# Kernel tuning notes

Hardware: AMD Instinct MI355X
Metric: run time of the kernel (lower is better)

Reference implementation:

```python
import jax, jax.numpy as jnp
import numpy as np

B, S, D, M = 2, 4096, 128, 64

def _linear_init(key, shape, fan_in):
    bound = 1.0 / np.sqrt(fan_in)
    return jax.random.uniform(key, shape, jnp.float32, -bound, bound)

def setup_inputs() -> dict:
    key = jax.random.key(0)
    ks = jax.random.split(key, 18)
    x = jax.random.normal(ks[0], (B, S, D), jnp.float32)
    context = jax.random.normal(ks[1], (B, S, D), jnp.float32)
    # per-mechanism params (torch Linear semantics: y = x @ W.T + b)
    Wt = _linear_init(ks[2], (M, D, D), D)   # transform weight, laid out [m, in, out]
    bt = _linear_init(ks[3], (M, D), D)
    char = jax.random.normal(ks[4], (M, D), jnp.float32)  # characteristics [1,1,d] per mech
    Wg = _linear_init(ks[5], (M, D), D)      # timing_gate weight (out=1)
    bg = _linear_init(ks[6], (M,), D)
    Wv = _linear_init(ks[7], (M, D), D)      # victory_detector weight (out=1)
    bv = _linear_init(ks[8], (M,), D)
    O = jax.random.normal(ks[9], (M, M), jnp.float32) * 0.02  # overcoming matrix
    # selector: Linear(2D,2D) -> GELU -> Linear(2D,M)
    W1 = _linear_init(ks[10], (2 * D, 2 * D), 2 * D)
    b1 = _linear_init(ks[11], (2 * D,), 2 * D)
    W2 = _linear_init(ks[12], (2 * D, M), 2 * D)
    b2 = _linear_init(ks[13], (M,), 2 * D)
    # integrate: Linear(2D, D)
    Wi = _linear_init(ks[14], (2 * D, D), 2 * D)
    bi = _linear_init(ks[15], (D,), 2 * D)
    return {"x": x, "context": context, "Wt": Wt, "bt": bt, "char": char,
            "Wg": Wg, "bg": bg, "Wv": Wv, "bv": bv, "O": O,
            "W1": W1, "b1": b1, "W2": W2, "b2": b2, "Wi": Wi, "bi": bi}

def reference(x, context, Wt, bt, char, Wg, bg, Wv, bv, O, W1, b1, W2, b2, Wi, bi):
    # selection scores over mechanisms
    sel_in = jnp.concatenate([x, context], axis=-1)          # [b,s,2d]
    h = jax.nn.gelu(sel_in @ W1 + b1, approximate=False)
    selection_scores = jax.nn.softmax(h @ W2 + b2, axis=-1)  # [b,s,m]
    # all 64 mechanism nodes as one batched GEMM
    transformed = jnp.einsum('bsd,mde->bsme', x, Wt) + bt + char   # [b,s,m,d]
    timing = jax.nn.sigmoid(jnp.einsum('bsd,md->bsm', x, Wg) + bg)  # [b,s,m]
    victory = jax.nn.sigmoid(jnp.einsum('bsme,me->bsm', transformed, Wv) + bv)
    outputs = transformed * timing[..., None]                # [b,s,m,d]
    # strategic overcoming modulation: gate = 1 + tanh(scores @ O)
    gates = 1.0 + jnp.tanh(selection_scores @ O)             # [b,s,m]
    selected = jnp.einsum('bsme,bsm->bse', outputs, gates * selection_scores)
    victory_potential = jnp.sum(victory * selection_scores, axis=-1)  # [b,s]
    integrated = jnp.concatenate([x, selected], axis=-1) @ Wi + bi    # [b,s,d]
    return integrated, victory_potential
```

## Files before the change

### kernel.cpp

```cpp
#include <hip/hip_runtime.h>
#include <hip/hip_bf16.h>


typedef __bf16 bf16_t;
typedef __bf16 bf16x8 __attribute__((ext_vector_type(8)));
typedef float  f32x4  __attribute__((ext_vector_type(4)));

#define WS_WTT      0u
#define WS_W1T      2097152u
#define WS_W2T      2228224u
#define WS_OT       2260992u
#define WS_WG       2269184u
#define WS_U        2285568u
#define WS_CVEC     2301952u
#define WS_BCT      2302208u
#define WS_WIT      2318592u
#define WS_WT       2384128u
#define WS_SBIAS    4481280u
#define WS_SEL0     8675584u
#define WS_SEL1     12869888u

#define VP_OFF 1048576

__device__ __forceinline__ f32x4 mfma16(bf16x8 a, bf16x8 b, f32x4 c) {
  return __builtin_amdgcn_mfma_f32_16x16x32_bf16(a, b, c, 0, 0, 0);
}

__device__ __forceinline__ float erf_fast(float x) {
  float ax = fabsf(x);
  float t = 1.0f / (1.0f + 0.3275911f * ax);
  float p = t * (0.254829592f + t * (-0.284496736f + t * (1.421413741f +
            t * (-1.453152027f + t * 1.061405429f))));
  float y = 1.0f - p * __expf(-ax * ax);
  return copysignf(y, x);
}
__device__ __forceinline__ float gelu_fast(float v) {
  return 0.5f * v * (1.0f + erf_fast(v * 0.70710678118654752f));
}
__device__ __forceinline__ float tanh_fast(float x) {
  float xc = fminf(fmaxf(x, -15.f), 15.f);
  float e = __expf(2.0f * xc);
  return (e - 1.0f) / (e + 1.0f);
}
__device__ __forceinline__ float sigmoidf_(float v) {
  return 1.0f / (1.0f + __expf(-v));
}

__device__ __forceinline__ bf16x8 cvt8(float4 v0, float4 v1) {
  bf16x8 a;
  a[0] = (bf16_t)v0.x; a[1] = (bf16_t)v0.y; a[2] = (bf16_t)v0.z; a[3] = (bf16_t)v0.w;
  a[4] = (bf16_t)v1.x; a[5] = (bf16_t)v1.y; a[6] = (bf16_t)v1.z; a[7] = (bf16_t)v1.w;
  return a;
}

__global__ __launch_bounds__(256) void kprep(
    const float* __restrict__ Wt, const float* __restrict__ bt,
    const float* __restrict__ ch, const float* __restrict__ Wg,
    const float* __restrict__ Wv, const float* __restrict__ bv,
    const float* __restrict__ O, const float* __restrict__ W1,
    const float* __restrict__ W2, const float* __restrict__ Wi,
    char* __restrict__ ws)
{
  const int bid = blockIdx.x, tid = threadIdx.x;
  if (bid < 128) {
    const int m = bid >> 1, half = bid & 1;
    const float* wtm = Wt + m * 16384;
    bf16_t* wtt = (bf16_t*)(ws + WS_WTT) + m * 16384;
    const int ks = half * 2 + (tid >> 7), e = tid & 127;
    bf16_t tmp[32];
    #pragma unroll
    for (int dd = 0; dd < 32; ++dd)
      tmp[dd] = (bf16_t)wtm[(ks * 32 + dd) * 128 + e];
    bf16_t* dst = wtt + ks * 4096 + e * 32;
    #pragma unroll
    for (int g = 0; g < 4; ++g)
      *(bf16x8*)(dst + g * 8) = *(const bf16x8*)(tmp + g * 8);
  } else if (bid < 144) {
    int base = (bid - 128) * 256 + tid;
    int k = base >> 4, c0 = (base & 15) * 16;
    bf16_t* o = (bf16_t*)(ws + WS_W1T);
    #pragma unroll
    for (int j = 0; j < 16; ++j) o[(c0 + j) * 256 + k] = (bf16_t)W1[k * 256 + c0 + j];
  } else if (bid < 146) {
    int base = (bid - 144) * 256 + tid;
    int k = base >> 1, c0 = (base & 1) * 32;
    bf16_t* o = (bf16_t*)(ws + WS_W2T);
    #pragma unroll
    for (int j = 0; j < 32; ++j) o[(c0 + j) * 256 + k] = (bf16_t)W2[k * 64 + c0 + j];
  } else if (bid == 146) {
    int k = tid >> 2, c0 = (tid & 3) * 16;
    bf16_t* o = (bf16_t*)(ws + WS_OT);
    #pragma unroll
    for (int j = 0; j < 16; ++j) o[(c0 + j) * 64 + k] = (bf16_t)O[k * 64 + c0 + j];
  } else if (bid == 147) {
    bf16_t* o = (bf16_t*)(ws + WS_WG);
    #pragma unroll
    for (int j = 0; j < 32; ++j) o[tid * 32 + j] = (bf16_t)Wg[tid * 32 + j];
  } else if (bid == 148) {
    bf16_t* o = (bf16_t*)(ws + WS_BCT);
    #pragma unroll
    for (int i = 0; i < 4; ++i) {
      int task = tid + i * 256;
      int m = task >> 4, e0 = (task & 15) * 8;
      #pragma unroll
      for (int j = 0; j < 8; ++j)
        o[(e0 + j) * 64 + m] = (bf16_t)(bt[m * 128 + e0 + j] + ch[m * 128 + e0 + j]);
    }
  } else if (bid < 153) {
    int base = (bid - 149) * 256 + tid;
    int k = base >> 2, c0 = (base & 3) * 32;
    bf16_t* o = (bf16_t*)(ws + WS_WIT);
    #pragma unroll
    for (int j = 0; j < 32; ++j) o[(c0 + j) * 256 + k] = (bf16_t)Wi[k * 128 + c0 + j];
  } else if (bid < 185) {
    int task = (bid - 153) * 256 + tid;
    int m = task >> 7, d = task & 127;
    const float4* wp = (const float4*)(Wt + m * 16384 + d * 128);
    const float4* vp = (const float4*)(Wv + m * 128);
    float s = 0.f;
    #pragma unroll
    for (int i = 0; i < 32; ++i) {
      float4 a = wp[i], b = vp[i];
      s += a.x * b.x + a.y * b.y + a.z * b.z + a.w * b.w;
    }
    ((bf16_t*)(ws + WS_U))[m * 128 + d] = (bf16_t)s;
  } else {
    if (tid < 64) {
      int m = tid;
      const float4* bp = (const float4*)(bt + m * 128);
      const float4* cp = (const float4*)(ch + m * 128);
      const float4* vp = (const float4*)(Wv + m * 128);
      float s = bv[m];
      #pragma unroll
      for (int i = 0; i < 32; ++i) {
        float4 a = bp[i], c = cp[i], b = vp[i];
        s += (a.x + c.x) * b.x + (a.y + c.y) * b.y + (a.z + c.z) * b.z + (a.w + c.w) * b.w;
      }
      ((float*)(ws + WS_CVEC))[m] = s;
    }
  }
}

__global__ __launch_bounds__(256) void kselect(
    const float* __restrict__ x, const float* __restrict__ ctx,
    const float* __restrict__ b1, const float* __restrict__ b2,
    const float* __restrict__ bg,
    char* __restrict__ ws, float* __restrict__ out)
{
  __shared__ char sm[43008];
  bf16_t* hL      = (bf16_t*)sm;
  float*  scoresL = (float*)(sm + 16384);
  float*  wLT     = (float*)(sm + 24576);
  bf16_t* scbL    = (bf16_t*)(sm + 33792);
  bf16_t* wbL     = (bf16_t*)(sm + 37888);
  float*  vpL     = (float*)(sm + 41984);

  const int tid = threadIdx.x;
  const int lane = tid & 63, wq = tid >> 6;
  const int tb = blockIdx.x * 32;
  const int lr = lane & 15, lg = lane >> 4;
  const int lk = lg * 8, lj4 = lg * 4;

  const bf16_t* W1t = (const bf16_t*)(ws + WS_W1T);
  const bf16_t* W2t = (const bf16_t*)(ws + WS_W2T);
  const bf16_t* Ot  = (const bf16_t*)(ws + WS_OT);
  const bf16_t* Wgb = (const bf16_t*)(ws + WS_WG);
  const bf16_t* Ub  = (const bf16_t*)(ws + WS_U);
  const float*  cv  = (const float*)(ws + WS_CVEC);
  const bf16_t* bct = (const bf16_t*)(ws + WS_BCT);
  float* wT    = (float*)(ws + WS_WT);
  float* sbOut = (float*)(ws + WS_SBIAS);

  bf16x8 aX[2][4];
  #pragma unroll
  for (int rg = 0; rg < 2; ++rg) {
    const float* xr = x + (tb + rg * 16 + lr) * 128;
    #pragma unroll
    for (int ks = 0; ks < 4; ++ks)
      aX[rg][ks] = cvt8(*(const float4*)(xr + ks * 32 + lk),
                        *(const float4*)(xr + ks * 32 + lk + 4));
  }

  {
    f32x4 a1[4][2] = {{{0,0,0,0},{0,0,0,0}},{{0,0,0,0},{0,0,0,0}},
                      {{0,0,0,0},{0,0,0,0}},{{0,0,0,0},{0,0,0,0}}};
    #pragma unroll
    for (int ks = 0; ks < 8; ++ks) {
      bf16x8 af[2];
      if (ks < 4) {
        af[0] = aX[0][ks]; af[1] = aX[1][ks];
      } else {
        #pragma unroll
        for (int rg = 0; rg < 2; ++rg) {
          const float* cr = ctx + (tb + rg * 16 + lr) * 128 + (ks - 4) * 32 + lk;
          af[rg] = cvt8(*(const float4*)cr, *(const float4*)(cr + 4));
        }
      }
      #pragma unroll
      for (int cg = 0; cg < 4; ++cg) {
        bf16x8 b = *(const bf16x8*)(W1t + (wq * 64 + cg * 16 + lr) * 256 + ks * 32 + lk);
        a1[cg][0] = mfma16(af[0], b, a1[cg][0]);
        a1[cg][1] = mfma16(af[1], b, a1[cg][1]);
      }
    }
    #pragma unroll
    for (int cg = 0; cg < 4; ++cg) {
      int c = wq * 64 + cg * 16 + lr;
      float bb = b1[c];
      #pragma unroll
      for (int rg = 0; rg < 2; ++rg)
        #pragma unroll
        for (int j = 0; j < 4; ++j) {
          int r = rg * 16 + lj4 + j;
          float v = gelu_fast(a1[cg][rg][j] + bb);
          *(bf16_t*)((char*)hL + ((r * 512 + c * 2) ^ ((r & 7) << 4))) = (bf16_t)v;
        }
    }
  }
  __syncthreads();

  {
    int c = wq * 16 + lr;
    f32x4 l[2] = {{0,0,0,0},{0,0,0,0}};
    #pragma unroll
    for (int ks = 0; ks < 8; ++ks) {
      int k0 = ks * 32 + lk;
      bf16x8 b = *(const bf16x8*)(W2t + c * 256 + k0);
      #pragma unroll
      for (int rg = 0; rg < 2; ++rg) {
        int r = rg * 16 + lr;
        bf16x8 a = *(const bf16x8*)((char*)hL + ((r * 512 + k0 * 2) ^ ((r & 7) << 4)));
        l[rg] = mfma16(a, b, l[rg]);
      }
    }
    float bb = b2[c];
    #pragma unroll
    for (int rg = 0; rg < 2; ++rg)
      #pragma unroll
      for (int j = 0; j < 4; ++j)
        scoresL[(rg * 16 + lj4 + j) * 64 + c] = l[rg][j] + bb;
  }
  __syncthreads();

  {
    int row = tid >> 3, i = tid & 7;
    float v[8];
    #pragma unroll
    for (int j = 0; j < 8; ++j) v[j] = scoresL[row * 64 + i * 8 + j];
    float mx = v[0];
    #pragma unroll
    for (int j = 1; j < 8; ++j) mx = fmaxf(mx, v[j]);
    mx = fmaxf(mx, __shfl_xor(mx, 1));
    mx = fmaxf(mx, __shfl_xor(mx, 2));
    mx = fmaxf(mx, __shfl_xor(mx, 4));
    float sum = 0.f;
    #pragma unroll
    for (int j = 0; j < 8; ++j) { v[j] = __expf(v[j] - mx); sum += v[j]; }
    sum += __shfl_xor(sum, 1);
    sum += __shfl_xor(sum, 2);
    sum += __shfl_xor(sum, 4);
    float inv = 1.0f / sum;
    #pragma unroll
    for (int j = 0; j < 8; ++j) {
      float s = v[j] * inv;
      int cc = i * 8 + j;
      scoresL[row * 64 + cc] = s;
      *(bf16_t*)((char*)scbL + ((row * 128 + cc * 2) ^ ((row & 7) << 4))) = (bf16_t)s;
    }
  }
  __syncthreads();

  {
    const int c = wq * 16 + lr;
    f32x4 g[2] = {{0,0,0,0},{0,0,0,0}};
    #pragma unroll
    for (int ks = 0; ks < 2; ++ks) {
      int k0 = ks * 32 + lk;
      bf16x8 b = *(const bf16x8*)(Ot + c * 64 + k0);
      #pragma unroll
      for (int rg = 0; rg < 2; ++rg) {
        int r = rg * 16 + lr;
        bf16x8 a = *(const bf16x8*)((char*)scbL + ((r * 128 + k0 * 2) ^ ((r & 7) << 4)));
        g[rg] = mfma16(a, b, g[rg]);
      }
    }
    f32x4 t[2] = {{0,0,0,0},{0,0,0,0}};
    f32x4 v[2] = {{0,0,0,0},{0,0,0,0}};
    #pragma unroll
    for (int ks = 0; ks < 4; ++ks) {
      bf16x8 bT = *(const bf16x8*)(Wgb + c * 128 + ks * 32 + lk);
      bf16x8 bV = *(const bf16x8*)(Ub  + c * 128 + ks * 32 + lk);
      #pragma unroll
      for (int rg = 0; rg < 2; ++rg) {
        t[rg] = mfma16(aX[rg][ks], bT, t[rg]);
        v[rg] = mfma16(aX[rg][ks], bV, v[rg]);
      }
    }
    float bgc = bg[c], cvc = cv[c];
    #pragma unroll
    for (int rg = 0; rg < 2; ++rg)
      #pragma unroll
      for (int j = 0; j < 4; ++j) {
        int r = rg * 16 + lj4 + j;
        float gate = 1.0f + tanh_fast(g[rg][j]);
        float tim  = sigmoidf_(t[rg][j] + bgc);
        float vic  = sigmoidf_(v[rg][j] + cvc);
        float sc   = scoresL[r * 64 + c];
        float w    = gate * sc * tim;
        wLT[c * 36 + r] = w;
        *(bf16_t*)((char*)wbL + ((r * 128 + c * 2) ^ ((r & 7) << 4))) = (bf16_t)w;
        float pv = vic * sc;
        pv += __shfl_xor(pv, 1); pv += __shfl_xor(pv, 2);
        pv += __shfl_xor(pv, 4); pv += __shfl_xor(pv, 8);
        if (lr == 0) vpL[r * 4 + wq] = pv;
      }
  }
  __syncthreads();

  if (tid < 32) {
    float s = vpL[tid * 4 + 0] + vpL[tid * 4 + 1] + vpL[tid * 4 + 2] + vpL[tid * 4 + 3];
    out[VP_OFF + tb + tid] = s;
  }
  {
    int m = tid >> 2, r0 = (tid & 3) * 8;
    float4 v0 = *(const float4*)&wLT[m * 36 + r0];
    float4 v1 = *(const float4*)&wLT[m * 36 + r0 + 4];
    *(float4*)&wT[m * 8192 + tb + r0] = v0;
    *(float4*)&wT[m * 8192 + tb + r0 + 4] = v1;
  }
  #pragma unroll
  for (int cg = 0; cg < 2; ++cg) {
    int eg = wq * 32 + cg * 16 + lr;
    f32x4 s[2] = {{0,0,0,0},{0,0,0,0}};
    #pragma unroll
    for (int ks = 0; ks < 2; ++ks) {
      int k0 = ks * 32 + lk;
      bf16x8 b = *(const bf16x8*)(bct + eg * 64 + k0);
      #pragma unroll
      for (int rg = 0; rg < 2; ++rg) {
        int r = rg * 16 + lr;
        bf16x8 a = *(const bf16x8*)((char*)wbL + ((r * 128 + k0 * 2) ^ ((r & 7) << 4)));
        s[rg] = mfma16(a, b, s[rg]);
      }
    }
    #pragma unroll
    for (int rg = 0; rg < 2; ++rg)
      #pragma unroll
      for (int j = 0; j < 4; ++j)
        sbOut[(tb + rg * 16 + lj4 + j) * 128 + eg] = s[rg][j];
  }
}

__device__ __forceinline__ void loadF(bf16x8 (&F)[4], const char* bbase, int mm) {
  const char* p = bbase + mm * 32768;
  F[0] = *(const bf16x8*)(p);
  F[1] = *(const bf16x8*)(p + 8192);
  F[2] = *(const bf16x8*)(p + 16384);
  F[3] = *(const bf16x8*)(p + 24576);
}

__device__ __forceinline__ void stepM(const bf16x8 (&F)[4], const float* wrow,
                                      const bf16x8 (&aX)[4][4], f32x4 (&acc)[4], int lj4) {
  f32x4 y[4] = {{0,0,0,0},{0,0,0,0},{0,0,0,0},{0,0,0,0}};
  #pragma unroll
  for (int ks = 0; ks < 4; ++ks) {
    y[0] = mfma16(aX[0][ks], F[ks], y[0]);
    y[1] = mfma16(aX[1][ks], F[ks], y[1]);
    y[2] = mfma16(aX[2][ks], F[ks], y[2]);
    y[3] = mfma16(aX[3][ks], F[ks], y[3]);
  }
  #pragma unroll
  for (int rg = 0; rg < 4; ++rg) {
    f32x4 wv = *(const f32x4*)(wrow + rg * 16 + lj4);
    #pragma unroll
    for (int jj = 0; jj < 4; ++jj)
      acc[rg][jj] += wv[jj] * y[rg][jj];
  }
}

__global__ __launch_bounds__(256, 2) void kmech(
    const float* __restrict__ x, char* __restrict__ ws)
{
  __shared__ float wmT[32 * 68];
  const int tid = threadIdx.x;
  const int lane = tid & 63, wq = tid >> 6;
  const int b = blockIdx.x;
  const int tile = b >> 2, eh = (b >> 1) & 1, mh = b & 1;
  const int tb = tile * 64;
  const int lr = lane & 15, lg = lane >> 4;
  const int lk = lg * 8, lj4 = lg * 4;

  const char* wttc = (const char*)(ws + WS_WTT);
  const float* wT = (const float*)(ws + WS_WT);
  float* selOut = (float*)(ws + (mh ? WS_SEL1 : WS_SEL0));

  {
    int mm = tid >> 3, r0 = (tid & 7) * 8;
    const float* src = wT + (mh * 32 + mm) * 8192 + tb + r0;
    float4 a = *(const float4*)src, c = *(const float4*)(src + 4);
    *(float4*)&wmT[mm * 68 + r0] = a;
    *(float4*)&wmT[mm * 68 + r0 + 4] = c;
  }
  bf16x8 aX[4][4];
  #pragma unroll
  for (int rg = 0; rg < 4; ++rg) {
    const float* xr = x + (tb + rg * 16 + lr) * 128;
    #pragma unroll
    for (int ks = 0; ks < 4; ++ks)
      aX[rg][ks] = cvt8(*(const float4*)(xr + ks * 32 + lk),
                        *(const float4*)(xr + ks * 32 + lk + 4));
  }
  f32x4 acc[4] = {{0,0,0,0},{0,0,0,0},{0,0,0,0},{0,0,0,0}};
  __syncthreads();

  const char* bbase = wttc + (size_t)(mh * 32) * 32768
                    + (size_t)(((eh * 64 + wq * 16 + lr) * 32 + lg * 8) * 2);
  bf16x8 F0[4], F1[4], F2[4], F3[4];
  loadF(F0, bbase, 0);
  loadF(F1, bbase, 1);
  loadF(F2, bbase, 2);

  #pragma unroll
  for (int it = 0; it < 8; ++it) {
    const int base = it * 4;
    const int n3 = base + 3;
    const int n4 = base + 4 > 31 ? 31 : base + 4;
    const int n5 = base + 5 > 31 ? 31 : base + 5;
    const int n6 = base + 6 > 31 ? 31 : base + 6;
    loadF(F3, bbase, n3);
    stepM(F0, &wmT[(base + 0) * 68], aX, acc, lj4);
    loadF(F0, bbase, n4);
    stepM(F1, &wmT[(base + 1) * 68], aX, acc, lj4);
    loadF(F1, bbase, n5);
    stepM(F2, &wmT[(base + 2) * 68], aX, acc, lj4);
    loadF(F2, bbase, n6);
    stepM(F3, &wmT[(base + 3) * 68], aX, acc, lj4);
  }

  #pragma unroll
  for (int rg = 0; rg < 4; ++rg)
    #pragma unroll
    for (int j = 0; j < 4; ++j)
      selOut[(tb + rg * 16 + lj4 + j) * 128 + eh * 64 + wq * 16 + lr] = acc[rg][j];
}

__global__ __launch_bounds__(256) void kinteg(
    const float* __restrict__ x, const float* __restrict__ bi,
    const char* __restrict__ ws, float* __restrict__ out)
{
  const int tid = threadIdx.x;
  const int lane = tid & 63, wq = tid >> 6;
  const int tb = blockIdx.x * 32;
  const int lr = lane & 15, lg = lane >> 4;
  const int lk = lg * 8, lj4 = lg * 4;
  const bf16_t* Wit = (const bf16_t*)(ws + WS_WIT);
  const float* s0 = (const float*)(ws + WS_SEL0);
  const float* s1 = (const float*)(ws + WS_SEL1);
  const float* sb = (const float*)(ws + WS_SBIAS);

  bf16x8 aF[2][8];
  #pragma unroll
  for (int rg = 0; rg < 2; ++rg) {
    int t = tb + rg * 16 + lr;
    #pragma unroll
    for (int ks = 0; ks < 4; ++ks) {
      const float* src = x + t * 128 + ks * 32 + lk;
      aF[rg][ks] = cvt8(*(const float4*)src, *(const float4*)(src + 4));
    }
    #pragma unroll
    for (int ks = 0; ks < 4; ++ks) {
      int idx = t * 128 + ks * 32 + lk;
      float4 a0 = *(const float4*)(s0 + idx);
      float4 a1 = *(const float4*)(s1 + idx);
      float4 a2 = *(const float4*)(sb + idx);
      float4 b0 = *(const float4*)(s0 + idx + 4);
      float4 b1 = *(const float4*)(s1 + idx + 4);
      float4 b2 = *(const float4*)(sb + idx + 4);
      float4 u; u.x = a0.x + a1.x + a2.x; u.y = a0.y + a1.y + a2.y;
      u.z = a0.z + a1.z + a2.z; u.w = a0.w + a1.w + a2.w;
      float4 v; v.x = b0.x + b1.x + b2.x; v.y = b0.y + b1.y + b2.y;
      v.z = b0.z + b1.z + b2.z; v.w = b0.w + b1.w + b2.w;
      aF[rg][4 + ks] = cvt8(u, v);
    }
  }
  #pragma unroll
  for (int cg = 0; cg < 2; ++cg) {
    int c = wq * 32 + cg * 16 + lr;
    f32x4 a0 = {0,0,0,0}, a1 = {0,0,0,0};
    #pragma unroll
    for (int ks = 0; ks < 8; ++ks) {
      bf16x8 b = *(const bf16x8*)(Wit + c * 256 + ks * 32 + lk);
      a0 = mfma16(aF[0][ks], b, a0);
      a1 = mfma16(aF[1][ks], b, a1);
    }
    float bb = bi[c];
    #pragma unroll
    for (int j = 0; j < 4; ++j) {
      out[(tb + lj4 + j) * 128 + c] = a0[j] + bb;
      out[(tb + 16 + lj4 + j) * 128 + c] = a1[j] + bb;
    }
  }
}

extern "C" void kernel_launch(void* const* d_in, const int* in_sizes, int n_in,
                              void* d_out, int out_size, void* d_ws, size_t ws_size,
                              hipStream_t stream)
{
  (void)in_sizes; (void)n_in; (void)out_size; (void)ws_size;
  const float* x   = (const float*)d_in[0];
  const float* ctx = (const float*)d_in[1];
  const float* Wt  = (const float*)d_in[2];
  const float* bt  = (const float*)d_in[3];
  const float* ch  = (const float*)d_in[4];
  const float* Wg  = (const float*)d_in[5];
  const float* bg  = (const float*)d_in[6];
  const float* Wv  = (const float*)d_in[7];
  const float* bv  = (const float*)d_in[8];
  const float* O   = (const float*)d_in[9];
  const float* W1  = (const float*)d_in[10];
  const float* b1  = (const float*)d_in[11];
  const float* W2  = (const float*)d_in[12];
  const float* b2  = (const float*)d_in[13];
  const float* Wi  = (const float*)d_in[14];
  const float* bi  = (const float*)d_in[15];
  float* out = (float*)d_out;
  char* ws = (char*)d_ws;

  kprep<<<186, 256, 0, stream>>>(Wt, bt, ch, Wg, Wv, bv, O, W1, W2, Wi, ws);
  kselect<<<256, 256, 0, stream>>>(x, ctx, b1, b2, bg, ws, out);
  kmech<<<512, 256, 0, stream>>>(x, ws);
  kinteg<<<256, 256, 0, stream>>>(x, bi, ws, out);
}
```

Baseline: 152.7 us.

## Restructure mechanism kernel: larger token tiles, in-block mechanism split-K reduction

```diff
diff --git a/kernel.cpp b/kernel.cpp
--- a/kernel.cpp
+++ b/kernel.cpp
@@ -17,8 +17,7 @@
 #define WS_WIT      2318592u
 #define WS_WT       2384128u
 #define WS_SBIAS    4481280u
-#define WS_SEL0     8675584u
-#define WS_SEL1     12869888u
+#define WS_SEL      8675584u
 
 #define VP_OFF 1048576
 
@@ -351,97 +350,132 @@
   }
 }
 
-__device__ __forceinline__ void loadF(bf16x8 (&F)[4], const char* bbase, int mm) {
-  const char* p = bbase + mm * 32768;
+__device__ __forceinline__ void loadF4(bf16x8 (&F)[4], const char* bbase, int m) {
+  const char* p = bbase + m * 32768;
   F[0] = *(const bf16x8*)(p);
   F[1] = *(const bf16x8*)(p + 8192);
   F[2] = *(const bf16x8*)(p + 16384);
   F[3] = *(const bf16x8*)(p + 24576);
 }
 
-__device__ __forceinline__ void stepM(const bf16x8 (&F)[4], const float* wrow,
-                                      const bf16x8 (&aX)[4][4], f32x4 (&acc)[4], int lj4) {
-  f32x4 y[4] = {{0,0,0,0},{0,0,0,0},{0,0,0,0},{0,0,0,0}};
+__device__ __forceinline__ void loadG(bf16x8 (&F)[4][4], const char* bbase, int mg) {
   #pragma unroll
-  for (int ks = 0; ks < 4; ++ks) {
-    y[0] = mfma16(aX[0][ks], F[ks], y[0]);
-    y[1] = mfma16(aX[1][ks], F[ks], y[1]);
-    y[2] = mfma16(aX[2][ks], F[ks], y[2]);
-    y[3] = mfma16(aX[3][ks], F[ks], y[3]);
-  }
+  for (int j = 0; j < 4; ++j) loadF4(F[j], bbase, mg + j);
+}
+
+__device__ __forceinline__ void groupStep(const bf16x8 (&F)[4][4], int mg,
+                                          const bf16_t* xL, const float* wmT,
+                                          f32x4 (&acc)[8], int lr, int lg, int lj4) {
   #pragma unroll
-  for (int rg = 0; rg < 4; ++rg) {
-    f32x4 wv = *(const f32x4*)(wrow + rg * 16 + lj4);
-    #pragma unroll
-    for (int jj = 0; jj < 4; ++jj)
-      acc[rg][jj] += wv[jj] * y[rg][jj];
-  }
-}
-
-__global__ __launch_bounds__(256, 2) void kmech(
+  for (int rg = 0; rg < 8; ++rg) {
+    const int r = rg * 16 + lr;
+    const int rx = (r & 7) << 4;
+    bf16x8 a0 = *(const bf16x8*)((const char*)xL + ((r * 256 +   0 + lg * 16) ^ rx));
+    bf16x8 a1 = *(const bf16x8*)((const char*)xL + ((r * 256 +  64 + lg * 16) ^ rx));
+    bf16x8 a2 = *(const bf16x8*)((const char*)xL + ((r * 256 + 128 + lg * 16) ^ rx));
+    bf16x8 a3 = *(const bf16x8*)((const char*)xL + ((r * 256 + 192 + lg * 16) ^ rx));
+    #pragma unroll
+    for (int J = 0; J < 4; ++J) {
+      f32x4 y = {0.f, 0.f, 0.f, 0.f};
+      y = mfma16(a0, F[J][0], y);
+      y = mfma16(a1, F[J][1], y);
+      y = mfma16(a2, F[J][2], y);
+      y = mfma16(a3, F[J][3], y);
+      f32x4 wv = *(const f32x4*)(wmT + (mg + J) * 132 + rg * 16 + lj4);
+      #pragma unroll
+      for (int jj = 0; jj < 4; ++jj)
+        acc[rg][jj] += wv[jj] * y[jj];
+    }
+  }
+}
+
+__global__ __launch_bounds__(512, 2) void kmech(
     const float* __restrict__ x, char* __restrict__ ws)
 {
-  __shared__ float wmT[32 * 68];
+  __shared__ char sm[66560];
+  bf16_t* xL  = (bf16_t*)sm;
+  float*  wmT = (float*)(sm + 32768);
+  float*  scr = (float*)sm;
+
   const int tid = threadIdx.x;
-  const int lane = tid & 63, wq = tid >> 6;
-  const int b = blockIdx.x;
-  const int tile = b >> 2, eh = (b >> 1) & 1, mh = b & 1;
-  const int tb = tile * 64;
+  const int lane = tid & 63, wid = tid >> 6;
+  const int es = wid & 1;
+  const int mq = wid >> 1;
+  const int tile = blockIdx.x >> 2, esl = blockIdx.x & 3;
+  const int tb = tile * 128;
   const int lr = lane & 15, lg = lane >> 4;
-  const int lk = lg * 8, lj4 = lg * 4;
-
-  const char* wttc = (const char*)(ws + WS_WTT);
-  const float* wT = (const float*)(ws + WS_WT);
-  float* selOut = (float*)(ws + (mh ? WS_SEL1 : WS_SEL0));
-
-  {
-    int mm = tid >> 3, r0 = (tid & 7) * 8;
-    const float* src = wT + (mh * 32 + mm) * 8192 + tb + r0;
-    float4 a = *(const float4*)src, c = *(const float4*)(src + 4);
-    *(float4*)&wmT[mm * 68 + r0] = a;
-    *(float4*)&wmT[mm * 68 + r0 + 4] = c;
-  }
-  bf16x8 aX[4][4];
-  #pragma unroll
-  for (int rg = 0; rg < 4; ++rg) {
-    const float* xr = x + (tb + rg * 16 + lr) * 128;
-    #pragma unroll
-    for (int ks = 0; ks < 4; ++ks)
-      aX[rg][ks] = cvt8(*(const float4*)(xr + ks * 32 + lk),
-                        *(const float4*)(xr + ks * 32 + lk + 4));
-  }
-  f32x4 acc[4] = {{0,0,0,0},{0,0,0,0},{0,0,0,0},{0,0,0,0}};
-  __syncthreads();
-
-  const char* bbase = wttc + (size_t)(mh * 32) * 32768
-                    + (size_t)(((eh * 64 + wq * 16 + lr) * 32 + lg * 8) * 2);
-  bf16x8 F0[4], F1[4], F2[4], F3[4];
-  loadF(F0, bbase, 0);
-  loadF(F1, bbase, 1);
-  loadF(F2, bbase, 2);
-
-  #pragma unroll
-  for (int it = 0; it < 8; ++it) {
-    const int base = it * 4;
-    const int n3 = base + 3;
-    const int n4 = base + 4 > 31 ? 31 : base + 4;
-    const int n5 = base + 5 > 31 ? 31 : base + 5;
-    const int n6 = base + 6 > 31 ? 31 : base + 6;
-    loadF(F3, bbase, n3);
-    stepM(F0, &wmT[(base + 0) * 68], aX, acc, lj4);
-    loadF(F0, bbase, n4);
-    stepM(F1, &wmT[(base + 1) * 68], aX, acc, lj4);
-    loadF(F1, bbase, n5);
-    stepM(F2, &wmT[(base + 2) * 68], aX, acc, lj4);
-    loadF(F2, bbase, n6);
-    stepM(F3, &wmT[(base + 3) * 68], aX, acc, lj4);
-  }
-
-  #pragma unroll
-  for (int rg = 0; rg < 4; ++rg)
-    #pragma unroll
-    for (int j = 0; j < 4; ++j)
-      selOut[(tb + rg * 16 + lj4 + j) * 128 + eh * 64 + wq * 16 + lr] = acc[rg][j];
+  const int lj4 = lg * 4;
+  const int eg = esl * 32 + es * 16 + lr;
+
+  {
+    int r = tid >> 2, c0 = (tid & 3) * 32;
+    const float* xr = x + (tb + r) * 128 + c0;
+    #pragma unroll
+    for (int k = 0; k < 4; ++k) {
+      bf16x8 v = cvt8(*(const float4*)(xr + k * 8), *(const float4*)(xr + k * 8 + 4));
+      *(bf16x8*)((char*)xL + ((r * 256 + (c0 + k * 8) * 2) ^ ((r & 7) << 4))) = v;
+    }
+  }
+  {
+    int m = tid >> 3, t0 = (tid & 7) * 16;
+    const float* src = (const float*)(ws + WS_WT) + m * 8192 + tb + t0;
+    #pragma unroll
+    for (int k = 0; k < 4; ++k)
+      *(float4*)&wmT[m * 132 + t0 + k * 4] = *(const float4*)(src + k * 4);
+  }
+  f32x4 acc[8];
+  if (mq == 0) {
+    const float* sb = (const float*)(ws + WS_SBIAS);
+    #pragma unroll
+    for (int rg = 0; rg < 8; ++rg)
+      #pragma unroll
+      for (int j = 0; j < 4; ++j)
+        acc[rg][j] = sb[(tb + rg * 16 + lj4 + j) * 128 + eg];
+  } else {
+    #pragma unroll
+    for (int rg = 0; rg < 8; ++rg) acc[rg] = (f32x4){0.f, 0.f, 0.f, 0.f};
+  }
+  __syncthreads();
+
+  const char* bbase = (const char*)(ws + WS_WTT) + (size_t)((eg * 32 + lg * 8) * 2);
+  const int m0 = mq * 16;
+
+  bf16x8 FA[4][4], FB[4][4];
+  loadG(FA, bbase, m0);
+  loadG(FB, bbase, m0 + 4);
+  groupStep(FA, m0,      xL, wmT, acc, lr, lg, lj4);
+  loadG(FA, bbase, m0 + 8);
+  groupStep(FB, m0 + 4,  xL, wmT, acc, lr, lg, lj4);
+  loadG(FB, bbase, m0 + 12);
+  groupStep(FA, m0 + 8,  xL, wmT, acc, lr, lg, lj4);
+  groupStep(FB, m0 + 12, xL, wmT, acc, lr, lg, lj4);
+
+  __syncthreads();
+  if (mq != 0) {
+    float* buf = scr + (es * 3 + mq - 1) * 2112;
+    #pragma unroll
+    for (int rg = 0; rg < 8; ++rg)
+      *(f32x4*)&buf[lr * 132 + rg * 16 + lj4] = acc[rg];
+  }
+  __syncthreads();
+  if (mq == 0) {
+    float* sel = (float*)(ws + WS_SEL);
+    const float* b0 = scr + (es * 3 + 0) * 2112;
+    const float* b1 = scr + (es * 3 + 1) * 2112;
+    const float* b2 = scr + (es * 3 + 2) * 2112;
+    #pragma unroll
+    for (int rg = 0; rg < 8; ++rg) {
+      f32x4 v = acc[rg];
+      f32x4 p0 = *(const f32x4*)&b0[lr * 132 + rg * 16 + lj4];
+      f32x4 p1 = *(const f32x4*)&b1[lr * 132 + rg * 16 + lj4];
+      f32x4 p2 = *(const f32x4*)&b2[lr * 132 + rg * 16 + lj4];
+      #pragma unroll
+      for (int j = 0; j < 4; ++j) {
+        float o = v[j] + p0[j] + p1[j] + p2[j];
+        sel[(tb + rg * 16 + lj4 + j) * 128 + eg] = o;
+      }
+    }
+  }
 }
 
 __global__ __launch_bounds__(256) void kinteg(
@@ -454,9 +488,7 @@
   const int lr = lane & 15, lg = lane >> 4;
   const int lk = lg * 8, lj4 = lg * 4;
   const bf16_t* Wit = (const bf16_t*)(ws + WS_WIT);
-  const float* s0 = (const float*)(ws + WS_SEL0);
-  const float* s1 = (const float*)(ws + WS_SEL1);
-  const float* sb = (const float*)(ws + WS_SBIAS);
+  const float* sel = (const float*)(ws + WS_SEL);
 
   bf16x8 aF[2][8];
   #pragma unroll
@@ -469,18 +501,8 @@
     }
     #pragma unroll
     for (int ks = 0; ks < 4; ++ks) {
-      int idx = t * 128 + ks * 32 + lk;
-      float4 a0 = *(const float4*)(s0 + idx);
-      float4 a1 = *(const float4*)(s1 + idx);
-      float4 a2 = *(const float4*)(sb + idx);
-      float4 b0 = *(const float4*)(s0 + idx + 4);
-      float4 b1 = *(const float4*)(s1 + idx + 4);
-      float4 b2 = *(const float4*)(sb + idx + 4);
-      float4 u; u.x = a0.x + a1.x + a2.x; u.y = a0.y + a1.y + a2.y;
-      u.z = a0.z + a1.z + a2.z; u.w = a0.w + a1.w + a2.w;
-      float4 v; v.x = b0.x + b1.x + b2.x; v.y = b0.y + b1.y + b2.y;
-      v.z = b0.z + b1.z + b2.z; v.w = b0.w + b1.w + b2.w;
-      aF[rg][4 + ks] = cvt8(u, v);
+      const float* src = sel + t * 128 + ks * 32 + lk;
+      aF[rg][4 + ks] = cvt8(*(const float4*)src, *(const float4*)(src + 4));
     }
   }
   #pragma unroll
@@ -528,6 +550,6 @@
 
   kprep<<<186, 256, 0, stream>>>(Wt, bt, ch, Wg, Wv, bv, O, W1, W2, Wi, ws);
   kselect<<<256, 256, 0, stream>>>(x, ctx, b1, b2, bg, ws, out);
-  kmech<<<512, 256, 0, stream>>>(x, ws);
+  kmech<<<256, 512, 0, stream>>>(x, ws);
   kinteg<<<256, 256, 0, stream>>>(x, bi, ws, out);
 }
```

Result: slower. 315.3 us (+106.5%).
